# Kernel tuning notes

Measured on AMD Instinct MI355X. Metric: run time of the kernel, lower is better.

## Reference

```python
import jax, jax.numpy as jnp
import numpy as np

EMBED = 1024
DFF = 4096


def _layernorm(x, g, b, eps=1e-5):
    mu = jnp.mean(x, axis=-1, keepdims=True)
    var = jnp.var(x, axis=-1, keepdims=True)
    return (x - mu) * jax.lax.rsqrt(var + eps) * g + b


def setup_inputs() -> dict:
    key = jax.random.key(0)
    ks = jax.random.split(key, 14)
    s = 1.0 / np.sqrt(EMBED)
    sf = 1.0 / np.sqrt(DFF)
    d = {
        "src": jax.random.normal(ks[0], (4, 2048, EMBED), dtype=jnp.float32),
        "Wq": jax.random.uniform(ks[1], (EMBED, EMBED), jnp.float32, -s, s),
        "bq": jnp.zeros((EMBED,), jnp.float32),
        "Wk": jax.random.uniform(ks[2], (EMBED, EMBED), jnp.float32, -s, s),
        "bk": jnp.zeros((EMBED,), jnp.float32),
        "Wv": jax.random.uniform(ks[3], (EMBED, EMBED), jnp.float32, -s, s),
        "bv": jnp.zeros((EMBED,), jnp.float32),
        "Wo": jax.random.uniform(ks[4], (EMBED, EMBED), jnp.float32, -s, s),
        "bo": jnp.zeros((EMBED,), jnp.float32),
        "W1": jax.random.uniform(ks[5], (EMBED, DFF), jnp.float32, -s, s),
        "b1": jnp.zeros((DFF,), jnp.float32),
        "W2": jax.random.uniform(ks[6], (DFF, EMBED), jnp.float32, -sf, sf),
        "b2": jnp.zeros((EMBED,), jnp.float32),
        "g1": jnp.ones((EMBED,), jnp.float32),
        "be1": jnp.zeros((EMBED,), jnp.float32),
        "g2": jnp.ones((EMBED,), jnp.float32),
        "be2": jnp.zeros((EMBED,), jnp.float32),
    }
    return d


def reference(src, Wq, bq, Wk, bk, Wv, bv, Wo, bo, W1, b1, W2, b2, g1, be1, g2, be2):
    # Q/K/V projections: [b, s, d]
    Q = src @ Wq + bq
    K = src @ Wk + bk
    V = src @ Wv + bv
    # Single-head, UNSCALED attention (faithful to source: no 1/sqrt(d), num_heads unused)
    scores = jnp.einsum("bqd,bkd->bqk", Q, K)  # [b, s, s]
    weights = jax.nn.softmax(scores, axis=-1)
    attn = jnp.einsum("bqk,bkd->bqd", weights, V)
    attn = attn @ Wo + bo
    x = _layernorm(src + attn, g1, be1)
    ff = jax.nn.relu(x @ W1 + b1) @ W2 + b2
    return _layernorm(x + ff, g2, be2)
```

## Files before the change

kernel.cpp:

```cpp
#include <hip/hip_runtime.h>
#include <stdint.h>

typedef unsigned short u16;
typedef _Float16 v8h __attribute__((ext_vector_type(8)));
typedef float v4f __attribute__((ext_vector_type(4)));

static __device__ __forceinline__ float h2f(u16 u) {
    union { u16 s; _Float16 h; } v; v.s = u; return (float)v.h;
}
static __device__ __forceinline__ u16 f2h(float f) {
    union { u16 s; _Float16 h; } v; v.h = (_Float16)f; return v.s;
}

static __device__ __forceinline__ void gload_lds16(const u16* g, const u16* l) {
    __builtin_amdgcn_global_load_lds(
        (const __attribute__((address_space(1))) uint32_t*)(uintptr_t)g,
        (__attribute__((address_space(3))) uint32_t*)(uintptr_t)l,
        16, 0, 0);
}

__global__ __launch_bounds__(256) void cvt_f16(const float* __restrict__ in,
                                               u16* __restrict__ out, int n8) {
    const int i = blockIdx.x * 256 + threadIdx.x;
    if (i >= n8) return;
    const float4 a = ((const float4*)in)[2 * i];
    const float4 b = ((const float4*)in)[2 * i + 1];
    u16 o[8] = {f2h(a.x), f2h(a.y), f2h(a.z), f2h(a.w),
                f2h(b.x), f2h(b.y), f2h(b.z), f2h(b.w)};
    *(uint4*)(out + (size_t)i * 8) = *(const uint4*)o;
}

__global__ __launch_bounds__(256) void transpose_all(
    const float* __restrict__ Wq, const float* __restrict__ Wk,
    const float* __restrict__ Wv, const float* __restrict__ Wo,
    const float* __restrict__ W1, const float* __restrict__ W2,
    u16* __restrict__ WqkvT, u16* __restrict__ WoT,
    u16* __restrict__ W1T, u16* __restrict__ W2T)
{
    int t = blockIdx.x;
    const float* in; u16* out; long ldi, ldo; int xt;
    if (t < 1024)      {            in = Wq; out = WqkvT;               ldi = 1024; ldo = 1024; xt = 32; }
    else if (t < 2048) { t -= 1024; in = Wk; out = WqkvT + 1024*1024;   ldi = 1024; ldo = 1024; xt = 32; }
    else if (t < 3072) { t -= 2048; in = Wv; out = WqkvT + 2*1024*1024; ldi = 1024; ldo = 1024; xt = 32; }
    else if (t < 4096) { t -= 3072; in = Wo; out = WoT;                 ldi = 1024; ldo = 1024; xt = 32; }
    else if (t < 8192) { t -= 4096; in = W1; out = W1T;                 ldi = 4096; ldo = 1024; xt = 128; }
    else               { t -= 8192; in = W2; out = W2T;                 ldi = 1024; ldo = 4096; xt = 32; }
    const int c0 = (t % xt) * 32, r0 = (t / xt) * 32;
    __shared__ float tile[32][33];
    for (int i = threadIdx.y; i < 32; i += 8)
        tile[i][threadIdx.x] = in[(long)(r0 + i) * ldi + c0 + threadIdx.x];
    __syncthreads();
    for (int i = threadIdx.y; i < 32; i += 8)
        out[(long)(c0 + i) * ldo + r0 + threadIdx.x] = f2h(tile[threadIdx.x][i]);
}

template<int OMODE, int BIAS, bool RELU, int NX, int NY, int NZ>
__global__ __launch_bounds__(256) void gemm_f16(
    const u16* __restrict__ A, long lda, long Asb,
    const u16* __restrict__ B, long ldb, long Bsb,
    void* __restrict__ Cv, long ldc, long Csb, u16* __restrict__ C1,
    const float* __restrict__ bias, const float* __restrict__ bias2,
    const float* __restrict__ bias3, int K)
{
    static_assert((NY * NZ) % 8 == 0, "Y-band remap needs NY*NZ % 8 == 0");
    alignas(16) __shared__ u16 As[128 * 64];
    alignas(16) __shared__ u16 Bs[128 * 64];
    const int t = threadIdx.x;

    const int lin = blockIdx.x + NX * (blockIdx.y + NY * blockIdx.z);
    const int g = lin & 7;
    const int s = lin >> 3;
    const int xe = s % NX;
    const int yl = s / NX;
    const int Y = g * (NY * NZ / 8) + yl;
    const int ye = Y % NY;
    const long b = Y / NY;

    A += b * Asb; B += b * Bsb;
    const long m0 = (long)ye * 128;
    const long n0 = (long)xe * 128;
    const int lane = t & 63, wave = t >> 6;
    const int wm = (wave >> 1) * 64, wn = (wave & 1) * 64;
    const int l16 = lane & 15, quad = lane >> 4;

    const int rr = t >> 3;
    const int cg8 = ((t & 7) ^ ((t >> 3) & 7)) * 8;
    const int wv512 = wave * 512;

    long aofs[4], bofs[4];
#pragma unroll
    for (int p = 0; p < 4; ++p) {
        aofs[p] = (m0 + p * 32 + rr) * lda + cg8;
        bofs[p] = (n0 + p * 32 + rr) * ldb + cg8;
    }

    v4f acc[4][4];
#pragma unroll
    for (int i = 0; i < 4; ++i)
#pragma unroll
        for (int j = 0; j < 4; ++j)
            acc[i][j] = (v4f){0.f, 0.f, 0.f, 0.f};

    for (int k0 = 0; k0 < K; k0 += 64) {
        __syncthreads();
#pragma unroll
        for (int p = 0; p < 4; ++p) {
            gload_lds16(A + aofs[p] + k0, As + p * 2048 + wv512);
            gload_lds16(B + bofs[p] + k0, Bs + p * 2048 + wv512);
        }
        __syncthreads();

#pragma unroll
        for (int kk = 0; kk < 2; ++kk) {
            const int swz = ((kk * 4 + quad) ^ (l16 & 7)) * 8;
            v8h af[4], bfr[4];
#pragma unroll
            for (int i = 0; i < 4; ++i)
                af[i] = *(const v8h*)&As[(wm + i * 16 + l16) * 64 + swz];
#pragma unroll
            for (int j = 0; j < 4; ++j)
                bfr[j] = *(const v8h*)&Bs[(wn + j * 16 + l16) * 64 + swz];
#pragma unroll
            for (int i = 0; i < 4; ++i)
#pragma unroll
                for (int j = 0; j < 4; ++j)
                    acc[i][j] = __builtin_amdgcn_mfma_f32_16x16x32_f16(af[i], bfr[j], acc[i][j], 0, 0, 0);
        }
    }

    float bv[4];
#pragma unroll
    for (int j = 0; j < 4; ++j) {
        const long col = n0 + wn + j * 16 + l16;
        if (BIAS == 0) bv[j] = 0.f;
        else if (BIAS == 1) bv[j] = bias[col];
        else {
            const int sel = (int)(col >> 10);
            const float* bp = sel == 0 ? bias : (sel == 1 ? bias2 : bias3);
            bv[j] = bp[col & 1023];
        }
    }

    if (OMODE == 3 && n0 >= 2048) {
        const long bb = m0 >> 11, mb = m0 & 2047;
        u16* C = C1 + bb * Csb;
#pragma unroll
        for (int j = 0; j < 4; ++j) {
            const long col = n0 - 2048 + wn + j * 16 + l16;
            u16* pc = C + col * 2048 + mb + wm + quad * 4;
#pragma unroll
            for (int i = 0; i < 4; ++i) {
                u16 o[4];
#pragma unroll
                for (int r = 0; r < 4; ++r) {
                    float val = acc[i][j][r] + bv[j];
                    if (RELU) val = fmaxf(val, 0.f);
                    o[r] = f2h(val);
                }
                *(uint2*)(pc + i * 16) = *(const uint2*)o;
            }
        }
    } else {
        const long cb = b * ((OMODE == 3) ? 0 : Csb) + (m0 + wm + quad * 4) * ldc + (n0 + wn + l16);
        u16* p0 = (u16*)Cv + cb;
#pragma unroll
        for (int i = 0; i < 4; ++i)
#pragma unroll
            for (int r = 0; r < 4; ++r) {
                u16* prow = p0 + (long)(i * 16 + r) * ldc;
#pragma unroll
                for (int j = 0; j < 4; ++j) {
                    float val = acc[i][j][r] + bv[j];
                    if (RELU) val = fmaxf(val, 0.f);
                    prow[j * 16] = f2h(val);
                }
            }
    }
}

template<int OMODE, int BIAS, bool RELU, int NX, int NY, int NZ>
__global__ __launch_bounds__(512) void gemm256(
    const u16* __restrict__ A, long lda, long Asb,
    const u16* __restrict__ B, long ldb, long Bsb,
    void* __restrict__ Cv, long ldc, long Csb, u16* __restrict__ C1,
    const float* __restrict__ bias, const float* __restrict__ bias2,
    const float* __restrict__ bias3, int K)
{
    constexpr int NWG = NX * NY * NZ;
    static_assert(NWG % 8 == 0, "XCD swizzle needs nwg % 8 == 0");
    alignas(16) __shared__ u16 As[4 * 8192];
    alignas(16) __shared__ u16 Bs[4 * 8192];

    const int tid = threadIdx.x;
    const int lane = tid & 63, wave = tid >> 6;
    const int l16 = lane & 15, quad = lane >> 4;
    const int wm = wave >> 2;
    const int wn = wave & 3;

    const int lin = blockIdx.x;
    const int tl = (lin & 7) * (NWG / 8) + (lin >> 3);
    const int xe = tl % NX;
    const int ye = (tl / NX) % NY;
    const int zb = tl / (NX * NY);
    const long m0 = (long)ye * 256;
    const long n0 = (long)xe * 256;

    const u16* Aop = A + (long)zb * Asb;
    const u16* Bop = B + (long)zb * Bsb;

    const int srow = tid >> 2;
    const int sq = (tid & 3) ^ ((tid >> 3) & 3);
    const long gaofs0 = (m0 + srow) * lda + sq * 8;
    const long gaofs1 = gaofs0 + 128 * lda;
    const long gbofs0 = (n0 + srow) * ldb + sq * 8;
    const long gbofs1 = gbofs0 + 128 * ldb;
    const int wv512n = wave * 512;

    const int swzE = (quad ^ ((l16 >> 1) & 3)) * 8;
    const int aRow = (wm * 128 + l16) * 32 + swzE;
    const int bRow = (wn * 64 + l16) * 32 + swzE;

    v4f acc[8][4];
#pragma unroll
    for (int i = 0; i < 8; ++i)
#pragma unroll
        for (int j = 0; j < 4; ++j)
            acc[i][j] = (v4f){0.f, 0.f, 0.f, 0.f};
    v8h bf[4];

#define STAGE_A(RIDX, KP) do { \
        u16* lb_ = As + (RIDX) * 8192 + wv512n; \
        gload_lds16(Aop + gaofs0 + (KP), lb_); \
        gload_lds16(Aop + gaofs1 + (KP), lb_ + 4096); } while (0)
#define STAGE_B(RIDX, KP) do { \
        u16* lb_ = Bs + (RIDX) * 8192 + wv512n; \
        gload_lds16(Bop + gbofs0 + (KP), lb_); \
        gload_lds16(Bop + gbofs1 + (KP), lb_ + 4096); } while (0)

#define MF(CH, I, J) \
    acc[(CH) * 4 + (I)][J] = __builtin_amdgcn_mfma_f32_16x16x32_f16( \
        af##I, bf[J], acc[(CH) * 4 + (I)][J], 0, 0, 0)

#define PHASE(BUF, KH, CH, EVENW, ...) { \
        if (EVENW) asm volatile("s_waitcnt vmcnt(6)" ::: "memory"); \
        const u16* Ar_ = As + ((BUF) * 2 + (KH)) * 8192 + aRow + (CH) * 2048; \
        v8h af0 = *(const v8h*)(Ar_); \
        v8h af1 = *(const v8h*)(Ar_ + 512); \
        v8h af2 = *(const v8h*)(Ar_ + 1024); \
        v8h af3 = *(const v8h*)(Ar_ + 1536); \
        if ((CH) == 0) { \
            const u16* Br_ = Bs + ((BUF) * 2 + (KH)) * 8192 + bRow; \
            bf[0] = *(const v8h*)(Br_); \
            bf[1] = *(const v8h*)(Br_ + 512); \
            bf[2] = *(const v8h*)(Br_ + 1024); \
            bf[3] = *(const v8h*)(Br_ + 1536); \
        } \
        __VA_ARGS__; \
        __builtin_amdgcn_s_barrier(); \
        asm volatile("s_waitcnt lgkmcnt(0)" ::: "memory"); \
        __builtin_amdgcn_s_setprio(1); \
        MF(CH,0,0); MF(CH,0,1); MF(CH,0,2); MF(CH,0,3); \
        MF(CH,1,0); MF(CH,1,1); MF(CH,1,2); MF(CH,1,3); \
        MF(CH,2,0); MF(CH,2,1); MF(CH,2,2); MF(CH,2,3); \
        MF(CH,3,0); MF(CH,3,1); MF(CH,3,2); MF(CH,3,3); \
        __builtin_amdgcn_s_setprio(0); \
        __builtin_amdgcn_s_barrier(); \
    }

    STAGE_A(0, 0);  STAGE_B(0, 0);
    STAGE_A(1, 32); STAGE_B(1, 32);
    STAGE_A(2, 64); STAGE_B(2, 64);
    asm volatile("s_waitcnt vmcnt(8)" ::: "memory");
    __builtin_amdgcn_s_barrier();

    const int NT = K >> 7;
#pragma unroll 1
    for (int t = 0; t < NT; ++t) {
        const bool nl = (t < NT - 1);
        const long kb = (long)t * 128;
        const long kp1 = kb + 96;
        const long kp2 = kb + 128;
        const long kp2b = kb + 160;
        const long kp3 = kb + 192;

        PHASE(0, 0, 0, false, STAGE_A(3, kp1))
        PHASE(0, 0, 1, true,  STAGE_B(3, kp1))
        PHASE(0, 1, 0, false, if (nl) STAGE_A(0, kp2))
        PHASE(0, 1, 1, true,  if (nl) STAGE_B(0, kp2))
        PHASE(1, 0, 0, false, if (nl) STAGE_A(1, kp2b))
        PHASE(1, 0, 1, true,  if (nl) STAGE_B(1, kp2b))
        PHASE(1, 1, 0, false, if (nl) STAGE_A(2, kp3))
        PHASE(1, 1, 1, true,  if (nl) STAGE_B(2, kp3))
    }

#undef PHASE
#undef MF
#undef STAGE_A
#undef STAGE_B

    float bv[4];
#pragma unroll
    for (int j = 0; j < 4; ++j) {
        const long col = n0 + wn * 64 + j * 16 + l16;
        if (BIAS == 0) bv[j] = 0.f;
        else if (BIAS == 1) bv[j] = bias[col];
        else {
            const int sel = (int)(col >> 10);
            const float* bp = sel == 0 ? bias : (sel == 1 ? bias2 : bias3);
            bv[j] = bp[col & 1023];
        }
    }

    if (OMODE == 3 && n0 >= 2048) {
        const long bb = m0 >> 11, mb = m0 & 2047;
        u16* C = C1 + bb * Csb;
#pragma unroll
        for (int j = 0; j < 4; ++j) {
            const long col = n0 - 2048 + wn * 64 + j * 16 + l16;
            u16* pc = C + col * 2048 + mb + wm * 128 + quad * 4;
#pragma unroll
            for (int i = 0; i < 8; ++i) {
                u16 o[4];
#pragma unroll
                for (int r = 0; r < 4; ++r) {
                    float val = acc[i][j][r] + bv[j];
                    if (RELU) val = fmaxf(val, 0.f);
                    o[r] = f2h(val);
                }
                *(uint2*)(pc + i * 16) = *(const uint2*)o;
            }
        }
    } else {
        const long cb = (OMODE == 3 ? 0 : (long)zb * Csb)
                      + (m0 + wm * 128 + quad * 4) * ldc + (n0 + wn * 64 + l16);
        u16* p0 = (u16*)Cv + cb;
#pragma unroll
        for (int i = 0; i < 8; ++i)
#pragma unroll
            for (int r = 0; r < 4; ++r) {
                u16* prow = p0 + (long)(i * 16 + r) * ldc;
#pragma unroll
                for (int j = 0; j < 4; ++j) {
                    float val = acc[i][j][r] + bv[j];
                    if (RELU) val = fmaxf(val, 0.f);
                    prow[j * 16] = f2h(val);
                }
            }
    }
}

__global__ __launch_bounds__(256) void softmax_rows(u16* __restrict__ S) {
    const long row = blockIdx.x;
    u16* p = S + row * 2048;
    const int t = threadIdx.x;
    float v[8];
    float mx = -1e30f;
#pragma unroll
    for (int i = 0; i < 8; ++i) { v[i] = h2f(p[t + i * 256]); mx = fmaxf(mx, v[i]); }
    __shared__ float red[256];
    red[t] = mx; __syncthreads();
    for (int off = 128; off > 0; off >>= 1) {
        if (t < off) red[t] = fmaxf(red[t], red[t + off]);
        __syncthreads();
    }
    mx = red[0]; __syncthreads();
    float sum = 0.f;
#pragma unroll
    for (int i = 0; i < 8; ++i) { v[i] = __expf(v[i] - mx); sum += v[i]; }
    red[t] = sum; __syncthreads();
    for (int off = 128; off > 0; off >>= 1) {
        if (t < off) red[t] += red[t + off];
        __syncthreads();
    }
    const float inv = 1.f / red[0];
#pragma unroll
    for (int i = 0; i < 8; ++i) p[t + i * 256] = f2h(v[i] * inv);
}

__global__ __launch_bounds__(256) void ln_one(
    const float* __restrict__ a, const u16* __restrict__ bb,
    const float* __restrict__ g, const float* __restrict__ be,
    u16* __restrict__ out16)
{
    const long base = (long)blockIdx.x * 1024;
    const int t = threadIdx.x;
    float v[4]; float s = 0.f, ss = 0.f;
#pragma unroll
    for (int i = 0; i < 4; ++i) {
        const int c = t + i * 256;
        const float x = a[base + c] + h2f(bb[base + c]);
        v[i] = x; s += x; ss += x * x;
    }
    __shared__ float rs[256], rss[256];
    rs[t] = s; rss[t] = ss; __syncthreads();
    for (int off = 128; off > 0; off >>= 1) {
        if (t < off) { rs[t] += rs[t + off]; rss[t] += rss[t + off]; }
        __syncthreads();
    }
    const float mean = rs[0] * (1.f / 1024.f);
    const float var = rss[0] * (1.f / 1024.f) - mean * mean;
    const float rstd = rsqrtf(var + 1e-5f);
#pragma unroll
    for (int i = 0; i < 4; ++i) {
        const int c = t + i * 256;
        out16[base + c] = f2h((v[i] - mean) * rstd * g[c] + be[c]);
    }
}

__global__ __launch_bounds__(256) void ln_two(
    const u16* __restrict__ a, const u16* __restrict__ bb,
    const float* __restrict__ g, const float* __restrict__ be,
    float* __restrict__ out)
{
    const long base = (long)blockIdx.x * 1024;
    const int t = threadIdx.x;
    float v[4]; float s = 0.f, ss = 0.f;
#pragma unroll
    for (int i = 0; i < 4; ++i) {
        const int c = t + i * 256;
        const float x = h2f(a[base + c]) + h2f(bb[base + c]);
        v[i] = x; s += x; ss += x * x;
    }
    __shared__ float rs[256], rss[256];
    rs[t] = s; rss[t] = ss; __syncthreads();
    for (int off = 128; off > 0; off >>= 1) {
        if (t < off) { rs[t] += rs[t + off]; rss[t] += rss[t + off]; }
        __syncthreads();
    }
    const float mean = rs[0] * (1.f / 1024.f);
    const float var = rss[0] * (1.f / 1024.f) - mean * mean;
    const float rstd = rsqrtf(var + 1e-5f);
#pragma unroll
    for (int i = 0; i < 4; ++i) {
        const int c = t + i * 256;
        out[base + c] = (v[i] - mean) * rstd * g[c] + be[c];
    }
}

extern "C" void kernel_launch(void* const* d_in, const int* in_sizes, int n_in,
                              void* d_out, int out_size, void* d_ws, size_t ws_size,
                              hipStream_t stream) {
    (void)in_sizes; (void)n_in; (void)out_size; (void)ws_size;
    constexpr long S = 2048, E = 1024, F = 4096, M = 8192;

    const float* src = (const float*)d_in[0];
    const float* Wq  = (const float*)d_in[1];
    const float* bq  = (const float*)d_in[2];
    const float* Wk  = (const float*)d_in[3];
    const float* bk  = (const float*)d_in[4];
    const float* Wv  = (const float*)d_in[5];
    const float* bv  = (const float*)d_in[6];
    const float* Wo  = (const float*)d_in[7];
    const float* bo  = (const float*)d_in[8];
    const float* W1  = (const float*)d_in[9];
    const float* b1  = (const float*)d_in[10];
    const float* W2  = (const float*)d_in[11];
    const float* b2  = (const float*)d_in[12];
    const float* g1  = (const float*)d_in[13];
    const float* be1 = (const float*)d_in[14];
    const float* g2  = (const float*)d_in[15];
    const float* be2 = (const float*)d_in[16];

    char* ws = (char*)d_ws;
    size_t off = 0;
    auto take = [&](size_t bytes) {
        char* p = ws + off;
        off += (bytes + 255) & ~(size_t)255;
        return p;
    };
    const size_t MB16 = 16777216;
    u16*   srcH  = (u16*)take(MB16);
    u16*   WqkvT = (u16*)take(3 * E * E * 2);
    u16*   WoT   = (u16*)take(E * E * 2);
    u16*   W1T   = (u16*)take(F * E * 2);
    u16*   W2T   = (u16*)take(E * F * 2);
    char*  B0    = take(2 * MB16);
    char*  B1    = take(MB16);
    char*  B2    = take(4ull * S * S * 4);
    char*  B3    = take(MB16);
    char*  B4    = take(MB16);

    u16*   QK    = (u16*)B0;
    u16*   VT    = (u16*)B1;
    u16*   Sh    = (u16*)B2;
    u16*   hf    = (u16*)B2;
    u16*   attn  = (u16*)B3;
    u16*   xh    = (u16*)B3;
    u16*   attnO = (u16*)B4;
    u16*   ffO   = (u16*)B4;

    dim3 blk(256), blk5(512), tb(32, 8);

    cvt_f16<<<dim3(M * E / 8 / 256), blk, 0, stream>>>(src, srcH, M * E / 8);

    transpose_all<<<dim3(12288), tb, 0, stream>>>(Wq, Wk, Wv, Wo, W1, W2,
                                                  WqkvT, WoT, W1T, W2T);

    gemm256<3, 3, false, 12, 32, 1><<<dim3(12 * 32), blk5, 0, stream>>>(
        srcH, E, 0, WqkvT, E, 0, QK, 2 * E, E * S, VT, bq, bk, bv, E);

    gemm256<0, 0, false, 8, 8, 4><<<dim3(8 * 8 * 4), blk5, 0, stream>>>(
        QK, 2 * E, S * 2 * E, QK + E, 2 * E, S * 2 * E,
        Sh, S, S * S, nullptr, nullptr, nullptr, nullptr, E);

    softmax_rows<<<dim3(M), blk, 0, stream>>>(Sh);

    gemm_f16<0, 0, false, 8, 16, 4><<<dim3(8, 16, 4), blk, 0, stream>>>(
        Sh, S, S * S, VT, S, E * S,
        attn, E, S * E, nullptr, nullptr, nullptr, nullptr, S);

    gemm_f16<0, 1, false, 8, 64, 1><<<dim3(8, 64, 1), blk, 0, stream>>>(
        attn, E, 0, WoT, E, 0, attnO, E, 0, nullptr, bo, nullptr, nullptr, E);

    ln_one<<<dim3(M), blk, 0, stream>>>(src, attnO, g1, be1, xh);

    gemm256<0, 1, true, 16, 32, 1><<<dim3(16 * 32), blk5, 0, stream>>>(
        xh, E, 0, W1T, E, 0, hf, F, 0, nullptr, b1, nullptr, nullptr, E);

    gemm_f16<0, 1, false, 8, 64, 1><<<dim3(8, 64, 1), blk, 0, stream>>>(
        hf, F, 0, W2T, F, 0, ffO, E, 0, nullptr, b2, nullptr, nullptr, F);

    ln_two<<<dim3(M), blk, 0, stream>>>(xh, ffO, g2, be2, (float*)d_out);
}
```

Baseline: 527.2 us.

## Replace 128x128 GEMMs with pipelined 256x128 gemm256n kernel for narrow GEMMs

```diff
diff --git a/kernel.cpp b/kernel.cpp
--- a/kernel.cpp
+++ b/kernel.cpp
@@ -52,130 +52,6 @@
     __syncthreads();
     for (int i = threadIdx.y; i < 32; i += 8)
         out[(long)(c0 + i) * ldo + r0 + threadIdx.x] = f2h(tile[threadIdx.x][i]);
-}
-
-template<int OMODE, int BIAS, bool RELU, int NX, int NY, int NZ>
-__global__ __launch_bounds__(256) void gemm_f16(
-    const u16* __restrict__ A, long lda, long Asb,
-    const u16* __restrict__ B, long ldb, long Bsb,
-    void* __restrict__ Cv, long ldc, long Csb, u16* __restrict__ C1,
-    const float* __restrict__ bias, const float* __restrict__ bias2,
-    const float* __restrict__ bias3, int K)
-{
-    static_assert((NY * NZ) % 8 == 0, "Y-band remap needs NY*NZ % 8 == 0");
-    alignas(16) __shared__ u16 As[128 * 64];
-    alignas(16) __shared__ u16 Bs[128 * 64];
-    const int t = threadIdx.x;
-
-    const int lin = blockIdx.x + NX * (blockIdx.y + NY * blockIdx.z);
-    const int g = lin & 7;
-    const int s = lin >> 3;
-    const int xe = s % NX;
-    const int yl = s / NX;
-    const int Y = g * (NY * NZ / 8) + yl;
-    const int ye = Y % NY;
-    const long b = Y / NY;
-
-    A += b * Asb; B += b * Bsb;
-    const long m0 = (long)ye * 128;
-    const long n0 = (long)xe * 128;
-    const int lane = t & 63, wave = t >> 6;
-    const int wm = (wave >> 1) * 64, wn = (wave & 1) * 64;
-    const int l16 = lane & 15, quad = lane >> 4;
-
-    const int rr = t >> 3;
-    const int cg8 = ((t & 7) ^ ((t >> 3) & 7)) * 8;
-    const int wv512 = wave * 512;
-
-    long aofs[4], bofs[4];
-#pragma unroll
-    for (int p = 0; p < 4; ++p) {
-        aofs[p] = (m0 + p * 32 + rr) * lda + cg8;
-        bofs[p] = (n0 + p * 32 + rr) * ldb + cg8;
-    }
-
-    v4f acc[4][4];
-#pragma unroll
-    for (int i = 0; i < 4; ++i)
-#pragma unroll
-        for (int j = 0; j < 4; ++j)
-            acc[i][j] = (v4f){0.f, 0.f, 0.f, 0.f};
-
-    for (int k0 = 0; k0 < K; k0 += 64) {
-        __syncthreads();
-#pragma unroll
-        for (int p = 0; p < 4; ++p) {
-            gload_lds16(A + aofs[p] + k0, As + p * 2048 + wv512);
-            gload_lds16(B + bofs[p] + k0, Bs + p * 2048 + wv512);
-        }
-        __syncthreads();
-
-#pragma unroll
-        for (int kk = 0; kk < 2; ++kk) {
-            const int swz = ((kk * 4 + quad) ^ (l16 & 7)) * 8;
-            v8h af[4], bfr[4];
-#pragma unroll
-            for (int i = 0; i < 4; ++i)
-                af[i] = *(const v8h*)&As[(wm + i * 16 + l16) * 64 + swz];
-#pragma unroll
-            for (int j = 0; j < 4; ++j)
-                bfr[j] = *(const v8h*)&Bs[(wn + j * 16 + l16) * 64 + swz];
-#pragma unroll
-            for (int i = 0; i < 4; ++i)
-#pragma unroll
-                for (int j = 0; j < 4; ++j)
-                    acc[i][j] = __builtin_amdgcn_mfma_f32_16x16x32_f16(af[i], bfr[j], acc[i][j], 0, 0, 0);
-        }
-    }
-
-    float bv[4];
-#pragma unroll
-    for (int j = 0; j < 4; ++j) {
-        const long col = n0 + wn + j * 16 + l16;
-        if (BIAS == 0) bv[j] = 0.f;
-        else if (BIAS == 1) bv[j] = bias[col];
-        else {
-            const int sel = (int)(col >> 10);
-            const float* bp = sel == 0 ? bias : (sel == 1 ? bias2 : bias3);
-            bv[j] = bp[col & 1023];
-        }
-    }
-
-    if (OMODE == 3 && n0 >= 2048) {
-        const long bb = m0 >> 11, mb = m0 & 2047;
-        u16* C = C1 + bb * Csb;
-#pragma unroll
-        for (int j = 0; j < 4; ++j) {
-            const long col = n0 - 2048 + wn + j * 16 + l16;
-            u16* pc = C + col * 2048 + mb + wm + quad * 4;
-#pragma unroll
-            for (int i = 0; i < 4; ++i) {
-                u16 o[4];
-#pragma unroll
-                for (int r = 0; r < 4; ++r) {
-                    float val = acc[i][j][r] + bv[j];
-                    if (RELU) val = fmaxf(val, 0.f);
-                    o[r] = f2h(val);
-                }
-                *(uint2*)(pc + i * 16) = *(const uint2*)o;
-            }
-        }
-    } else {
-        const long cb = b * ((OMODE == 3) ? 0 : Csb) + (m0 + wm + quad * 4) * ldc + (n0 + wn + l16);
-        u16* p0 = (u16*)Cv + cb;
-#pragma unroll
-        for (int i = 0; i < 4; ++i)
-#pragma unroll
-            for (int r = 0; r < 4; ++r) {
-                u16* prow = p0 + (long)(i * 16 + r) * ldc;
-#pragma unroll
-                for (int j = 0; j < 4; ++j) {
-                    float val = acc[i][j][r] + bv[j];
-                    if (RELU) val = fmaxf(val, 0.f);
-                    prow[j * 16] = f2h(val);
-                }
-            }
-    }
 }
 
 template<int OMODE, int BIAS, bool RELU, int NX, int NY, int NZ>
@@ -276,21 +152,20 @@
     const int NT = K >> 7;
 #pragma unroll 1
     for (int t = 0; t < NT; ++t) {
-        const bool nl = (t < NT - 1);
         const long kb = (long)t * 128;
         const long kp1 = kb + 96;
-        const long kp2 = kb + 128;
-        const long kp2b = kb + 160;
-        const long kp3 = kb + 192;
+        long kp2  = kb + 128; if (kp2  >= K) kp2  = 0;
+        long kp2b = kb + 160; if (kp2b >= K) kp2b = 0;
+        long kp3  = kb + 192; if (kp3  >= K) kp3  = 0;
 
         PHASE(0, 0, 0, false, STAGE_A(3, kp1))
         PHASE(0, 0, 1, true,  STAGE_B(3, kp1))
-        PHASE(0, 1, 0, false, if (nl) STAGE_A(0, kp2))
-        PHASE(0, 1, 1, true,  if (nl) STAGE_B(0, kp2))
-        PHASE(1, 0, 0, false, if (nl) STAGE_A(1, kp2b))
-        PHASE(1, 0, 1, true,  if (nl) STAGE_B(1, kp2b))
-        PHASE(1, 1, 0, false, if (nl) STAGE_A(2, kp3))
-        PHASE(1, 1, 1, true,  if (nl) STAGE_B(2, kp3))
+        PHASE(0, 1, 0, false, STAGE_A(0, kp2))
+        PHASE(0, 1, 1, true,  STAGE_B(0, kp2))
+        PHASE(1, 0, 0, false, STAGE_A(1, kp2b))
+        PHASE(1, 0, 1, true,  STAGE_B(1, kp2b))
+        PHASE(1, 1, 0, false, STAGE_A(2, kp3))
+        PHASE(1, 1, 1, true,  STAGE_B(2, kp3))
     }
 
 #undef PHASE
@@ -341,6 +216,171 @@
                 u16* prow = p0 + (long)(i * 16 + r) * ldc;
 #pragma unroll
                 for (int j = 0; j < 4; ++j) {
+                    float val = acc[i][j][r] + bv[j];
+                    if (RELU) val = fmaxf(val, 0.f);
+                    prow[j * 16] = f2h(val);
+                }
+            }
+    }
+}
+
+template<int OMODE, int BIAS, bool RELU, int NX, int NY, int NZ>
+__global__ __launch_bounds__(512) void gemm256n(
+    const u16* __restrict__ A, long lda, long Asb,
+    const u16* __restrict__ B, long ldb, long Bsb,
+    void* __restrict__ Cv, long ldc, long Csb, u16* __restrict__ C1,
+    const float* __restrict__ bias, const float* __restrict__ bias2,
+    const float* __restrict__ bias3, int K)
+{
+    constexpr int NWG = NX * NY * NZ;
+    static_assert(NWG % 8 == 0, "XCD swizzle needs nwg % 8 == 0");
+    alignas(16) __shared__ u16 As[4 * 8192];
+    alignas(16) __shared__ u16 Bs[4 * 4096];
+
+    const int tid = threadIdx.x;
+    const int lane = tid & 63, wave = tid >> 6;
+    const int l16 = lane & 15, quad = lane >> 4;
+    const int wm = wave >> 2;
+    const int wn = wave & 3;
+
+    const int lin = blockIdx.x;
+    const int tl = (lin & 7) * (NWG / 8) + (lin >> 3);
+    const int xe = tl % NX;
+    const int ye = (tl / NX) % NY;
+    const int zb = tl / (NX * NY);
+    const long m0 = (long)ye * 256;
+    const long n0 = (long)xe * 128;
+
+    const u16* Aop = A + (long)zb * Asb;
+    const u16* Bop = B + (long)zb * Bsb;
+
+    const int srow = tid >> 2;
+    const int sq = (tid & 3) ^ ((tid >> 3) & 3);
+    const long gaofs0 = (m0 + srow) * lda + sq * 8;
+    const long gaofs1 = gaofs0 + 128 * lda;
+    const long gbofs0 = (n0 + srow) * ldb + sq * 8;
+    const int wv512n = wave * 512;
+
+    const int swzE = (quad ^ ((l16 >> 1) & 3)) * 8;
+    const int aRow = (wm * 128 + l16) * 32 + swzE;
+    const int bRow = (wn * 32 + l16) * 32 + swzE;
+
+    v4f acc[8][2];
+#pragma unroll
+    for (int i = 0; i < 8; ++i)
+#pragma unroll
+        for (int j = 0; j < 2; ++j)
+            acc[i][j] = (v4f){0.f, 0.f, 0.f, 0.f};
+    v8h bf[2];
+
+#define STAGE_A(RIDX, KP) do { \
+        u16* lb_ = As + (RIDX) * 8192 + wv512n; \
+        gload_lds16(Aop + gaofs0 + (KP), lb_); \
+        gload_lds16(Aop + gaofs1 + (KP), lb_ + 4096); } while (0)
+#define STAGE_B(RIDX, KP) do { \
+        gload_lds16(Bop + gbofs0 + (KP), Bs + (RIDX) * 4096 + wv512n); } while (0)
+
+#define MF(CH, I, J) \
+    acc[(CH) * 4 + (I)][J] = __builtin_amdgcn_mfma_f32_16x16x32_f16( \
+        af##I, bf[J], acc[(CH) * 4 + (I)][J], 0, 0, 0)
+
+#define PHASE(BUF, KH, CH, EVENW, ...) { \
+        if (EVENW) asm volatile("s_waitcnt vmcnt(5)" ::: "memory"); \
+        const u16* Ar_ = As + ((BUF) * 2 + (KH)) * 8192 + aRow + (CH) * 2048; \
+        v8h af0 = *(const v8h*)(Ar_); \
+        v8h af1 = *(const v8h*)(Ar_ + 512); \
+        v8h af2 = *(const v8h*)(Ar_ + 1024); \
+        v8h af3 = *(const v8h*)(Ar_ + 1536); \
+        if ((CH) == 0) { \
+            const u16* Br_ = Bs + ((BUF) * 2 + (KH)) * 4096 + bRow; \
+            bf[0] = *(const v8h*)(Br_); \
+            bf[1] = *(const v8h*)(Br_ + 512); \
+        } \
+        __VA_ARGS__; \
+        __builtin_amdgcn_s_barrier(); \
+        asm volatile("s_waitcnt lgkmcnt(0)" ::: "memory"); \
+        __builtin_amdgcn_s_setprio(1); \
+        MF(CH,0,0); MF(CH,0,1); \
+        MF(CH,1,0); MF(CH,1,1); \
+        MF(CH,2,0); MF(CH,2,1); \
+        MF(CH,3,0); MF(CH,3,1); \
+        __builtin_amdgcn_s_setprio(0); \
+        __builtin_amdgcn_s_barrier(); \
+    }
+
+    STAGE_A(0, 0);  STAGE_B(0, 0);
+    STAGE_A(1, 32); STAGE_B(1, 32);
+    STAGE_A(2, 64); STAGE_B(2, 64);
+    asm volatile("s_waitcnt vmcnt(6)" ::: "memory");
+    __builtin_amdgcn_s_barrier();
+
+    const int NT = K >> 7;
+#pragma unroll 1
+    for (int t = 0; t < NT; ++t) {
+        const long kb = (long)t * 128;
+        const long kp1 = kb + 96;
+        long kp2  = kb + 128; if (kp2  >= K) kp2  = 0;
+        long kp2b = kb + 160; if (kp2b >= K) kp2b = 0;
+        long kp3  = kb + 192; if (kp3  >= K) kp3  = 0;
+
+        PHASE(0, 0, 0, false, STAGE_A(3, kp1))
+        PHASE(0, 0, 1, true,  STAGE_B(3, kp1))
+        PHASE(0, 1, 0, false, STAGE_A(0, kp2))
+        PHASE(0, 1, 1, true,  STAGE_B(0, kp2))
+        PHASE(1, 0, 0, false, STAGE_A(1, kp2b))
+        PHASE(1, 0, 1, true,  STAGE_B(1, kp2b))
+        PHASE(1, 1, 0, false, STAGE_A(2, kp3))
+        PHASE(1, 1, 1, true,  STAGE_B(2, kp3))
+    }
+
+#undef PHASE
+#undef MF
+#undef STAGE_A
+#undef STAGE_B
+
+    float bv[2];
+#pragma unroll
+    for (int j = 0; j < 2; ++j) {
+        const long col = n0 + wn * 32 + j * 16 + l16;
+        if (BIAS == 0) bv[j] = 0.f;
+        else if (BIAS == 1) bv[j] = bias[col];
+        else {
+            const int sel = (int)(col >> 10);
+            const float* bp = sel == 0 ? bias : (sel == 1 ? bias2 : bias3);
+            bv[j] = bp[col & 1023];
+        }
+    }
+
+    if (OMODE == 3 && n0 >= 2048) {
+        const long bb = m0 >> 11, mb = m0 & 2047;
+        u16* C = C1 + bb * Csb;
+#pragma unroll
+        for (int j = 0; j < 2; ++j) {
+            const long col = n0 - 2048 + wn * 32 + j * 16 + l16;
+            u16* pc = C + col * 2048 + mb + wm * 128 + quad * 4;
+#pragma unroll
+            for (int i = 0; i < 8; ++i) {
+                u16 o[4];
+#pragma unroll
+                for (int r = 0; r < 4; ++r) {
+                    float val = acc[i][j][r] + bv[j];
+                    if (RELU) val = fmaxf(val, 0.f);
+                    o[r] = f2h(val);
+                }
+                *(uint2*)(pc + i * 16) = *(const uint2*)o;
+            }
+        }
+    } else {
+        const long cb = (OMODE == 3 ? 0 : (long)zb * Csb)
+                      + (m0 + wm * 128 + quad * 4) * ldc + (n0 + wn * 32 + l16);
+        u16* p0 = (u16*)Cv + cb;
+#pragma unroll
+        for (int i = 0; i < 8; ++i)
+#pragma unroll
+            for (int r = 0; r < 4; ++r) {
+                u16* prow = p0 + (long)(i * 16 + r) * ldc;
+#pragma unroll
+                for (int j = 0; j < 2; ++j) {
                     float val = acc[i][j][r] + bv[j];
                     if (RELU) val = fmaxf(val, 0.f);
                     prow[j * 16] = f2h(val);
@@ -496,7 +536,7 @@
     transpose_all<<<dim3(12288), tb, 0, stream>>>(Wq, Wk, Wv, Wo, W1, W2,
                                                   WqkvT, WoT, W1T, W2T);
 
-    gemm256<3, 3, false, 12, 32, 1><<<dim3(12 * 32), blk5, 0, stream>>>(
+    gemm256n<3, 3, false, 24, 32, 1><<<dim3(24 * 32), blk5, 0, stream>>>(
         srcH, E, 0, WqkvT, E, 0, QK, 2 * E, E * S, VT, bq, bk, bv, E);
 
     gemm256<0, 0, false, 8, 8, 4><<<dim3(8 * 8 * 4), blk5, 0, stream>>>(
@@ -505,11 +545,11 @@
 
     softmax_rows<<<dim3(M), blk, 0, stream>>>(Sh);
 
-    gemm_f16<0, 0, false, 8, 16, 4><<<dim3(8, 16, 4), blk, 0, stream>>>(
+    gemm256n<0, 0, false, 8, 8, 4><<<dim3(8 * 8 * 4), blk5, 0, stream>>>(
         Sh, S, S * S, VT, S, E * S,
         attn, E, S * E, nullptr, nullptr, nullptr, nullptr, S);
 
-    gemm_f16<0, 1, false, 8, 64, 1><<<dim3(8, 64, 1), blk, 0, stream>>>(
+    gemm256n<0, 1, false, 8, 32, 1><<<dim3(8 * 32), blk5, 0, stream>>>(
         attn, E, 0, WoT, E, 0, attnO, E, 0, nullptr, bo, nullptr, nullptr, E);
 
     ln_one<<<dim3(M), blk, 0, stream>>>(src, attnO, g1, be1, xh);
@@ -517,7 +557,7 @@
     gemm256<0, 1, true, 16, 32, 1><<<dim3(16 * 32), blk5, 0, stream>>>(
         xh, E, 0, W1T, E, 0, hf, F, 0, nullptr, b1, nullptr, nullptr, E);
 
-    gemm_f16<0, 1, false, 8, 64, 1><<<dim3(8, 64, 1), blk, 0, stream>>>(
+    gemm256n<0, 1, false, 8, 32, 1><<<dim3(8 * 32), blk5, 0, stream>>>(
         hf, F, 0, W2T, F, 0, ffO, E, 0, nullptr, b2, nullptr, nullptr, F);
 
     ln_two<<<dim3(M), blk, 0, stream>>>(xh, ffO, g2, be2, (float*)d_out);
```

After: 508.6 us. -3.5%, faster.
